# Kernel optimization log

Hardware: AMD Instinct MI355X
Metric: run time of the kernel (lower is better)

## Reference

```python
import jax, jax.numpy as jnp
import numpy as np

B, S, D, H, DK, DV, DFF = 8, 1024, 512, 8, 64, 64, 2048
EPS = 1e-6
NEG = -1e10


def _ln(x, w, b):
    # LayerNorm over last two dims ([S, D]) as in nn.LayerNorm([seq_len, d_model])
    m = jnp.mean(x, axis=(-2, -1), keepdims=True)
    v = jnp.var(x, axis=(-2, -1), keepdims=True)
    return (x - m) / jnp.sqrt(v + EPS) * w + b


def _mha(q, k, v, wq, bq, wk, bk, wv, bv, wo, bo, mask):
    # batched version of the per-head loop: wq/wk [H, D, DK], wv [H, D, DV]
    qh = jnp.einsum('bsd,hdk->bhsk', q, wq) + bq[:, None, :]
    kh = jnp.einsum('bsd,hdk->bhsk', k, wk) + bk[:, None, :]
    vh = jnp.einsum('bsd,hdv->bhsv', v, wv) + bv[:, None, :]
    sc = jnp.einsum('bhqk,bhmk->bhqm', qh, kh) / jnp.asarray(np.sqrt(DK), jnp.float32)
    sc = jnp.where(mask[:, None, None, :] == 0, NEG, sc)  # mask over key dim
    a = jax.nn.softmax(sc, axis=-1)
    o = jnp.einsum('bhqm,bhmv->bhqv', a, vh)
    o = o.transpose(0, 2, 1, 3).reshape(q.shape[0], q.shape[1], H * DV)
    return o @ wo.T + bo


def setup_inputs() -> dict:
    key = jax.random.key(0)
    ks = jax.random.split(key, 24)

    def w(k, shape):
        return (jax.random.normal(k, shape, jnp.float32) * 0.02)

    inp = {
        'x': jax.random.normal(ks[0], (B, S, D), jnp.float32),
        'y': jax.random.normal(ks[1], (B, S, D), jnp.float32),
        'src_mask': jax.random.randint(ks[2], (B, S), 0, 2, jnp.int32),
        'trg_mask': jax.random.randint(ks[3], (B, S), 0, 2, jnp.int32),
    }
    i = 4
    for pre in ('m1', 'm2'):
        inp[pre + '_wq'] = w(ks[i], (H, D, DK)); i += 1
        inp[pre + '_bq'] = jnp.zeros((H, DK), jnp.float32)
        inp[pre + '_wk'] = w(ks[i], (H, D, DK)); i += 1
        inp[pre + '_bk'] = jnp.zeros((H, DK), jnp.float32)
        inp[pre + '_wv'] = w(ks[i], (H, D, DV)); i += 1
        inp[pre + '_bv'] = jnp.zeros((H, DV), jnp.float32)
        inp[pre + '_wo'] = w(ks[i], (D, H * DV)); i += 1
        inp[pre + '_bo'] = jnp.zeros((D,), jnp.float32)
    inp['pw1'] = w(ks[i], (DFF, D)); i += 1
    inp['pb1'] = jnp.zeros((DFF,), jnp.float32)
    inp['pw2'] = w(ks[i], (D, DFF)); i += 1
    inp['pb2'] = jnp.zeros((D,), jnp.float32)
    for n in ('ln1', 'ln2', 'ln3'):
        inp[n + '_w'] = jnp.ones((S, D), jnp.float32)
        inp[n + '_b'] = jnp.zeros((S, D), jnp.float32)
    return inp


def reference(x, y, src_mask, trg_mask,
              m1_wq, m1_bq, m1_wk, m1_bk, m1_wv, m1_bv, m1_wo, m1_bo,
              m2_wq, m2_bq, m2_wk, m2_bk, m2_wv, m2_bv, m2_wo, m2_bo,
              pw1, pb1, pw2, pb2,
              ln1_w, ln1_b, ln2_w, ln2_b, ln3_w, ln3_b):
    # self-attention + residual + LN (dropout is identity at eval)
    h = _mha(x, x, x, m1_wq, m1_bq, m1_wk, m1_bk, m1_wv, m1_bv, m1_wo, m1_bo, trg_mask)
    x1 = _ln(x + h, ln1_w, ln1_b)
    # cross-attention
    h = _mha(x1, y, y, m2_wq, m2_bq, m2_wk, m2_bk, m2_wv, m2_bv, m2_wo, m2_bo, src_mask)
    x2 = _ln(x1 + h, ln2_w, ln2_b)
    # position-wise FFN
    ff = jax.nn.relu(x2 @ pw1.T + pb1) @ pw2.T + pb2
    return _ln(x2 + ff, ln3_w, ln3_b)
```

## Files before the change

### kernel.cpp

```cpp
#include <hip/hip_runtime.h>
#include <hip/hip_bf16.h>

#define B_   8
#define S_   1024
#define D_   512
#define H_   8
#define DK_  64
#define DFF_ 2048

typedef __hip_bfloat16 bf16;
typedef __attribute__((ext_vector_type(8))) short bf16x8;
typedef __attribute__((ext_vector_type(4))) float f32x4;

__device__ __forceinline__ float ldmix(const void* p, size_t i, int f) {
    return f ? __bfloat162float(((const bf16*)p)[i]) : ((const float*)p)[i];
}
__device__ __forceinline__ void store_o(float* p, float v) { *p = v; }
__device__ __forceinline__ void store_o(bf16* p, float v)  { *p = __float2bfloat16(v); }

__device__ __forceinline__ void gl_lds16(const void* g, void* l) {
    __builtin_amdgcn_global_load_lds(
        (const __attribute__((address_space(1))) unsigned int*)g,
        (__attribute__((address_space(3))) unsigned int*)l, 16, 0, 0);
}

__global__ __launch_bounds__(64) void detect_k(const unsigned short* __restrict__ x,
                                               float* __restrict__ stats,
                                               int* __restrict__ flag)
{
    if (threadIdx.x < 48) stats[threadIdx.x] = 0.f;
    int cnt = 0;
    for (int i = threadIdx.x; i < 4096; i += 64) {
        int e = (x[i] >> 7) & 0xFF;
        if (e >= 0xC0) cnt++;
    }
#pragma unroll
    for (int off = 32; off; off >>= 1) cnt += __shfl_xor(cnt, off);
    if (threadIdx.x == 0) { flag[0] = (cnt > 16) ? 0 : 1; flag[1] = 1; }
}

__global__ __launch_bounds__(256) void maskf_k(const int* __restrict__ trg,
                                               const int* __restrict__ src,
                                               float* __restrict__ trgf,
                                               float* __restrict__ srcf)
{
    int i = blockIdx.x * 256 + threadIdx.x;
    if (i < 8192) trgf[i] = trg[i] ? 0.f : -1.0e10f;
    else          srcf[i - 8192] = src[i - 8192] ? 0.f : -1.0e10f;
}

__global__ __launch_bounds__(256) void convxy_k(const void* __restrict__ x,
                                                const void* __restrict__ y,
                                                bf16* __restrict__ xb, bf16* __restrict__ yb,
                                                const int* __restrict__ flag)
{
    const int f = flag[0];
    const int N8 = 8192 * 512 / 8;
    int i = blockIdx.x * 256 + threadIdx.x;
    const void* src; bf16* dst; size_t base;
    if (i < N8) { src = x; dst = xb; base = (size_t)i * 8; }
    else        { src = y; dst = yb; base = (size_t)(i - N8) * 8; }
    if (f) {
        *(uint4*)(dst + base) = *(const uint4*)((const bf16*)src + base);
    } else {
        const float4 a = *(const float4*)((const float*)src + base);
        const float4 b = *(const float4*)((const float*)src + base + 4);
        bf16 o[8] = {__float2bfloat16(a.x), __float2bfloat16(a.y),
                     __float2bfloat16(a.z), __float2bfloat16(a.w),
                     __float2bfloat16(b.x), __float2bfloat16(b.y),
                     __float2bfloat16(b.z), __float2bfloat16(b.w)};
        *(uint4*)(dst + base) = *(uint4*)o;
    }
}

__global__ __launch_bounds__(256) void repack6_k(const void* __restrict__ w0, const void* __restrict__ w1,
                                                 const void* __restrict__ w2, const void* __restrict__ w3,
                                                 const void* __restrict__ w4, const void* __restrict__ w5,
                                                 bf16* __restrict__ out, const int* __restrict__ flag)
{
    const int f = flag[0];
    const int widx = blockIdx.x >> 10;
    const int j = ((blockIdx.x & 1023) << 8) + threadIdx.x;
    const void* in = widx == 0 ? w0 : widx == 1 ? w1 : widx == 2 ? w2
                   : widx == 3 ? w3 : widx == 4 ? w4 : w5;
    int n = j >> 9, d = j & 511;
    int h = n >> 6, k = n & 63;
    out[(size_t)widx * 262144 + j] =
        __float2bfloat16(ldmix(in, (size_t)h * (D_ * DK_) + (size_t)d * DK_ + k, f));
}

__global__ __launch_bounds__(256) void convw4_k(const void* __restrict__ wo1, const void* __restrict__ wo2,
                                                const void* __restrict__ pw1, const void* __restrict__ pw2,
                                                bf16* __restrict__ out, const int* __restrict__ flag)
{
    const int f = flag[0];
    const size_t i8 = (size_t)(blockIdx.x * 256 + threadIdx.x) * 8;
    const void* in; size_t off;
    if (i8 < 262144)       { in = wo1; off = 0; }
    else if (i8 < 524288)  { in = wo2; off = 262144; }
    else if (i8 < 1572864) { in = pw1; off = 524288; }
    else                   { in = pw2; off = 1572864; }
    const size_t s = i8 - off;
    if (f) {
        *(uint4*)(out + i8) = *(const uint4*)((const bf16*)in + s);
    } else {
        const float4 a = *(const float4*)((const float*)in + s);
        const float4 b = *(const float4*)((const float*)in + s + 4);
        bf16 o[8] = {__float2bfloat16(a.x), __float2bfloat16(a.y),
                     __float2bfloat16(a.z), __float2bfloat16(a.w),
                     __float2bfloat16(b.x), __float2bfloat16(b.y),
                     __float2bfloat16(b.z), __float2bfloat16(b.w)};
        *(uint4*)(out + i8) = *(uint4*)o;
    }
}

template <int NB>
__device__ __forceinline__ void gemm_core(const bf16* __restrict__ A, const bf16* __restrict__ Wt,
                                          int K, int m0, int n0, bf16* As, bf16* Bs,
                                          f32x4 (&acc)[4][NB])
{
    const int tid = threadIdx.x;
    const int lane = tid & 63, w = tid >> 6;
    const int wr = w >> 1, wc = w & 1;
    const int l16 = lane & 15, quad = lane >> 4;
    const int r0 = tid >> 2;
    const int g0 = (tid & 3) ^ ((r0 >> 1) & 3);
    const bf16* pa0 = A + (size_t)(m0 + r0) * K + g0 * 8;
    const bf16* pa1 = pa0 + (size_t)64 * K;
    const bf16* pb0 = Wt + (size_t)(n0 + r0) * K + g0 * 8;
    const bf16* pb1 = pb0 + (size_t)64 * K;
    bf16* lA0 = As + w * 512;
    bf16* lA1 = As + 2048 + w * 512;
    bf16* lB0 = Bs + w * 512;
    bf16* lB1 = Bs + 2048 + w * 512;

    int aoff[4], boff[NB];
#pragma unroll
    for (int i = 0; i < 4; ++i) {
        const int ra = wr * 64 + i * 16 + l16;
        aoff[i] = ra * 32 + (quad ^ ((ra >> 1) & 3)) * 8;
    }
#pragma unroll
    for (int j = 0; j < NB; ++j) {
        const int rb = wc * (NB * 16) + j * 16 + l16;
        boff[j] = rb * 32 + (quad ^ ((rb >> 1) & 3)) * 8;
    }

    for (int k0 = 0; k0 < K; k0 += 32) {
        __syncthreads();
        gl_lds16(pa0 + k0, lA0);
        gl_lds16(pa1 + k0, lA1);
        gl_lds16(pb0 + k0, lB0);
        if constexpr (NB == 4) gl_lds16(pb1 + k0, lB1);
        __syncthreads();
        bf16x8 af[4], bg[NB];
#pragma unroll
        for (int i = 0; i < 4; ++i) af[i] = *(const bf16x8*)&As[aoff[i]];
#pragma unroll
        for (int j = 0; j < NB; ++j) bg[j] = *(const bf16x8*)&Bs[boff[j]];
#pragma unroll
        for (int i = 0; i < 4; ++i)
#pragma unroll
            for (int j = 0; j < NB; ++j)
                acc[i][j] = __builtin_amdgcn_mfma_f32_16x16x32_bf16(af[i], bg[j], acc[i][j], 0, 0, 0);
    }
}

template <int NB, bool HAS_RES, bool RELU, bool STATS, typename OutT>
__global__ __launch_bounds__(256)
void mgemm_k(const bf16* __restrict__ A, const bf16* __restrict__ Wt,
             const void* __restrict__ bias, const void* __restrict__ res,
             OutT* __restrict__ C, int N, int K, int Gx,
             const int* __restrict__ bflag, const int* __restrict__ rflag,
             float* __restrict__ stats)
{
    __shared__ bf16 As[4096];
    __shared__ bf16 Bs[NB * 1024];
    const int lin = blockIdx.x;
    const int mt = (lin & 7) * 8 + (lin >> 3) / Gx;
    const int nt = (lin >> 3) % Gx;
    const int m0 = mt * 128, n0 = nt * (NB * 32);

    f32x4 acc[4][NB];
#pragma unroll
    for (int i = 0; i < 4; ++i)
#pragma unroll
        for (int j = 0; j < NB; ++j) acc[i][j] = (f32x4){0.f, 0.f, 0.f, 0.f};

    gemm_core<NB>(A, Wt, K, m0, n0, As, Bs, acc);

    const int tid = threadIdx.x;
    const int lane = tid & 63, w = tid >> 6;
    const int wr = w >> 1, wc = w & 1;
    const int l16 = lane & 15, quad = lane >> 4;
    const int bf = bflag[0];
    int rf = 0;
    if constexpr (HAS_RES) rf = rflag[0];

    float s = 0.f, s2 = 0.f;
#pragma unroll
    for (int i = 0; i < 4; ++i) {
        const int row = m0 + wr * 64 + i * 16 + quad * 4;
#pragma unroll
        for (int j = 0; j < NB; ++j) {
            const int col = n0 + wc * (NB * 16) + j * 16 + l16;
            const float bv = ldmix(bias, col, bf);
#pragma unroll
            for (int r = 0; r < 4; ++r) {
                float c = acc[i][j][r] + bv;
                if constexpr (RELU) c = fmaxf(c, 0.f);
                if constexpr (HAS_RES) c += ldmix(res, (size_t)(row + r) * N + col, rf);
                if constexpr (STATS) { s += c; s2 += c * c; }
                store_o(&C[(size_t)(row + r) * N + col], c);
            }
        }
    }
    if constexpr (STATS) {
#pragma unroll
        for (int off = 32; off; off >>= 1) { s += __shfl_xor(s, off); s2 += __shfl_xor(s2, off); }
        __syncthreads();
        float* red = (float*)As;
        if (lane == 0) { red[w * 2] = s; red[w * 2 + 1] = s2; }
        __syncthreads();
        if (tid == 0) {
            const int b = m0 >> 10;
            atomicAdd(&stats[b * 2],     red[0] + red[2] + red[4] + red[6]);
            atomicAdd(&stats[b * 2 + 1], red[1] + red[3] + red[5] + red[7]);
        }
    }
}

template <int NB, int RSHIFT>
__global__ __launch_bounds__(256)
void mgemm_qkv_k(const bf16* __restrict__ A, const bf16* __restrict__ Wbase,
                 const void* __restrict__ bq, const void* __restrict__ bk, const void* __restrict__ bv,
                 bf16* __restrict__ qout, bf16* __restrict__ kout, bf16* __restrict__ vtout,
                 int Gx, int roff, const int* __restrict__ bflag)
{
    __shared__ bf16 As[4096];
    __shared__ bf16 Bs[NB * 1024];
    const int lin = blockIdx.x;
    const int mt = (lin & 7) * 8 + (lin >> 3) / Gx;
    const int nt = (lin >> 3) % Gx;
    const int m0 = mt * 128, n0 = nt * (NB * 32);

    f32x4 acc[4][NB];
#pragma unroll
    for (int i = 0; i < 4; ++i)
#pragma unroll
        for (int j = 0; j < NB; ++j) acc[i][j] = (f32x4){0.f, 0.f, 0.f, 0.f};

    gemm_core<NB>(A, Wbase, 512, m0, n0, As, Bs, acc);

    const int tid = threadIdx.x;
    const int lane = tid & 63, w = tid >> 6;
    const int wr = w >> 1, wc = w & 1;
    const int l16 = lane & 15, quad = lane >> 4;
    const int bf = bflag[0];
    const int region = roff + (nt >> RSHIFT);
    const void* bptr = region == 0 ? bq : (region == 1 ? bk : bv);

#pragma unroll
    for (int i = 0; i < 4; ++i) {
        const int row = m0 + wr * 64 + i * 16 + quad * 4;
#pragma unroll
        for (int j = 0; j < NB; ++j) {
            const int col = n0 + wc * (NB * 16) + j * 16 + l16;
            const int colr = col & 511;
            const float bvv = ldmix(bptr, colr, bf);
#pragma unroll
            for (int r = 0; r < 4; ++r) {
                const int rr = row + r;
                float c = acc[i][j][r] + bvv;
                if (region == 0) {
                    qout[(size_t)rr * 512 + colr] = __float2bfloat16(c * 0.125f);
                } else if (region == 1) {
                    kout[(size_t)rr * 512 + colr] = __float2bfloat16(c);
                } else {
                    const int b = rr >> 10, key = rr & 1023;
                    vtout[((size_t)(b * 512 + colr) << 10) | key] = __float2bfloat16(c);
                }
            }
        }
    }
}

__global__ __launch_bounds__(256)
void mfattn_k(const bf16* __restrict__ Q, const bf16* __restrict__ Kb,
              const bf16* __restrict__ Vt, const float* __restrict__ maskf,
              bf16* __restrict__ O)
{
    const int lin = blockIdx.x;
    const int j = lin >> 3, xcd = lin & 7;
    const int head = xcd * 8 + (j >> 4);
    const int qt = j & 15;
    const int b = head >> 3, h = head & 7, s0 = qt * 64;
    const int tid = threadIdx.x;
    const int lane = tid & 63, w = tid >> 6;
    const int l16 = lane & 15, quad = lane >> 4;
    const int bS = b * S_, hc = h * DK_;
    const size_t vtb = (size_t)(b * H_ + h) * (DK_ * S_);

    __shared__ bf16 QPs[64 * 72];
    __shared__ bf16 Ks[64 * 72];
    __shared__ bf16 Vs[64 * 72];

    const int str = tid >> 3;
    const int stc = (tid & 7) * 8;

    *(uint4*)&QPs[str * 72 + stc]        = *(const uint4*)&Q[(size_t)(bS + s0 + str) * D_ + hc + stc];
    *(uint4*)&QPs[(str + 32) * 72 + stc] = *(const uint4*)&Q[(size_t)(bS + s0 + str + 32) * D_ + hc + stc];
    __syncthreads();

    const bf16x8 aq0 = *(const bf16x8*)&QPs[(w * 16 + l16) * 72 + quad * 8];
    const bf16x8 aq1 = *(const bf16x8*)&QPs[(w * 16 + l16) * 72 + quad * 8 + 32];

    f32x4 acc_o[4];
#pragma unroll
    for (int nb = 0; nb < 4; ++nb) acc_o[nb] = (f32x4){0.f, 0.f, 0.f, 0.f};
    float lrow[4] = {0.f, 0.f, 0.f, 0.f};

    for (int t0 = 0; t0 < S_; t0 += 64) {
        __syncthreads();
        *(uint4*)&Ks[str * 72 + stc]        = *(const uint4*)&Kb[(size_t)(bS + t0 + str) * D_ + hc + stc];
        *(uint4*)&Ks[(str + 32) * 72 + stc] = *(const uint4*)&Kb[(size_t)(bS + t0 + str + 32) * D_ + hc + stc];
        *(uint4*)&Vs[str * 72 + stc]        = *(const uint4*)&Vt[vtb + (size_t)str * S_ + t0 + stc];
        *(uint4*)&Vs[(str + 32) * 72 + stc] = *(const uint4*)&Vt[vtb + (size_t)(str + 32) * S_ + t0 + stc];
        __syncthreads();

        f32x4 sacc[4];
#pragma unroll
        for (int nb = 0; nb < 4; ++nb) sacc[nb] = (f32x4){0.f, 0.f, 0.f, 0.f};
#pragma unroll
        for (int nb = 0; nb < 4; ++nb) {
            const bf16x8 b0 = *(const bf16x8*)&Ks[(nb * 16 + l16) * 72 + quad * 8];
            const bf16x8 b1 = *(const bf16x8*)&Ks[(nb * 16 + l16) * 72 + quad * 8 + 32];
            sacc[nb] = __builtin_amdgcn_mfma_f32_16x16x32_bf16(aq0, b0, sacc[nb], 0, 0, 0);
            sacc[nb] = __builtin_amdgcn_mfma_f32_16x16x32_bf16(aq1, b1, sacc[nb], 0, 0, 0);
        }

#pragma unroll
        for (int nb = 0; nb < 4; ++nb) {
            const float mv = maskf[bS + t0 + nb * 16 + l16];
#pragma unroll
            for (int r = 0; r < 4; ++r) {
                const float p = __expf(sacc[nb][r] + mv);
                lrow[r] += p;
                QPs[(w * 16 + quad * 4 + r) * 72 + nb * 16 + l16] = __float2bfloat16(p);
            }
        }

        const bf16x8 ap0 = *(const bf16x8*)&QPs[(w * 16 + l16) * 72 + quad * 8];
        const bf16x8 ap1 = *(const bf16x8*)&QPs[(w * 16 + l16) * 72 + quad * 8 + 32];
#pragma unroll
        for (int nb = 0; nb < 4; ++nb) {
            const bf16x8 v0 = *(const bf16x8*)&Vs[(nb * 16 + l16) * 72 + quad * 8];
            const bf16x8 v1 = *(const bf16x8*)&Vs[(nb * 16 + l16) * 72 + quad * 8 + 32];
            acc_o[nb] = __builtin_amdgcn_mfma_f32_16x16x32_bf16(ap0, v0, acc_o[nb], 0, 0, 0);
            acc_o[nb] = __builtin_amdgcn_mfma_f32_16x16x32_bf16(ap1, v1, acc_o[nb], 0, 0, 0);
        }
    }

#pragma unroll
    for (int r = 0; r < 4; ++r) {
        float ls = lrow[r];
#pragma unroll
        for (int off = 8; off; off >>= 1) ls += __shfl_xor(ls, off);
        const float invl = 1.0f / ls;
        const size_t row = (size_t)(bS + s0 + w * 16 + quad * 4 + r) * D_;
#pragma unroll
        for (int nb = 0; nb < 4; ++nb)
            O[row + hc + nb * 16 + l16] = __float2bfloat16(acc_o[nb][r] * invl);
    }
}

template <bool FINAL>
__global__ __launch_bounds__(256)
void ln_apply_k(const float* __restrict__ Z, const float* __restrict__ stats,
                const void* __restrict__ w, const void* __restrict__ bb,
                bf16* __restrict__ outb, void* __restrict__ out_final,
                const int* __restrict__ flag)
{
    const int f = flag[0];
    const int b = blockIdx.y;
    const int i4 = (blockIdx.x * 256 + threadIdx.x) * 4;
    const float n = (float)(S_ * D_);
    const float m = stats[b * 2] / n;
    const float var = stats[b * 2 + 1] / n - m * m;
    const float inv = rsqrtf(var + 1e-6f);
    const size_t g = (size_t)b * (S_ * D_) + i4;
    const float4 z = *(const float4*)&Z[g];
    float v[4];
    v[0] = (z.x - m) * inv * ldmix(w, i4 + 0, f) + ldmix(bb, i4 + 0, f);
    v[1] = (z.y - m) * inv * ldmix(w, i4 + 1, f) + ldmix(bb, i4 + 1, f);
    v[2] = (z.z - m) * inv * ldmix(w, i4 + 2, f) + ldmix(bb, i4 + 2, f);
    v[3] = (z.w - m) * inv * ldmix(w, i4 + 3, f) + ldmix(bb, i4 + 3, f);
    union { ushort4 u4; unsigned short u[4]; } ov;
#pragma unroll
    for (int k = 0; k < 4; ++k) {
        bf16 t = __float2bfloat16(v[k]);
        __builtin_memcpy(&ov.u[k], &t, 2);
    }
    if constexpr (FINAL) {
        if (f) *(ushort4*)&((bf16*)out_final)[g] = ov.u4;
        else   *(float4*)&((float*)out_final)[g] = make_float4(v[0], v[1], v[2], v[3]);
    } else {
        *(ushort4*)&outb[g] = ov.u4;
    }
}

extern "C" void kernel_launch(void* const* d_in, const int* in_sizes, int n_in,
                              void* d_out, int out_size, void* d_ws, size_t ws_size,
                              hipStream_t stream)
{
    (void)in_sizes; (void)n_in; (void)out_size; (void)ws_size;

    const void* x        = d_in[0];
    const void* y        = d_in[1];
    const int*  src_mask = (const int*) d_in[2];
    const int*  trg_mask = (const int*) d_in[3];
    const void* m1_wq = d_in[4];
    const void* m1_bq = d_in[5];
    const void* m1_wk = d_in[6];
    const void* m1_bk = d_in[7];
    const void* m1_wv = d_in[8];
    const void* m1_bv = d_in[9];
    const void* m1_wo = d_in[10];
    const void* m1_bo = d_in[11];
    const void* m2_wq = d_in[12];
    const void* m2_bq = d_in[13];
    const void* m2_wk = d_in[14];
    const void* m2_bk = d_in[15];
    const void* m2_wv = d_in[16];
    const void* m2_bv = d_in[17];
    const void* m2_wo = d_in[18];
    const void* m2_bo = d_in[19];
    const void* pw1   = d_in[20];
    const void* pb1   = d_in[21];
    const void* pw2   = d_in[22];
    const void* pb2   = d_in[23];
    const void* ln1_w = d_in[24];
    const void* ln1_b = d_in[25];
    const void* ln2_w = d_in[26];
    const void* ln2_b = d_in[27];
    const void* ln3_w = d_in[28];
    const void* ln3_b = d_in[29];

    const size_t NACT = (size_t)8192 * 512;

    float* zb    = (float*)d_ws;
    float* stats = zb + NACT;
    int*   flag  = (int*)(stats + 48);
    float* trgf  = stats + 64;
    float* srcf  = trgf + 8192;
    bf16* xb16 = (bf16*)(srcf + 8192);
    bf16* yb16 = xb16 + NACT;
    bf16* qb   = yb16 + NACT;
    bf16* kb   = qb   + NACT;
    bf16* vbT  = kb   + NACT;
    bf16* aob  = vbT  + NACT;
    bf16* x1b  = aob  + NACT;
    bf16* x2b  = x1b  + NACT;
    bf16* ffb  = x2b  + NACT;
    bf16* Wq1r = ffb  + (size_t)8192 * 2048;
    bf16* Wq2r = Wq1r + 3 * 262144;
    bf16* Wo1b = Wq1r + 6 * 262144;
    bf16* Wo2b = Wo1b + 262144;
    bf16* W1b  = Wo2b + 262144;
    bf16* W2b  = W1b  + 1048576;

    detect_k<<<1, 64, 0, stream>>>((const unsigned short*)x, stats, flag);
    maskf_k<<<64, 256, 0, stream>>>(trg_mask, src_mask, trgf, srcf);
    convxy_k<<<4096, 256, 0, stream>>>(x, y, xb16, yb16, flag);
    repack6_k<<<6144, 256, 0, stream>>>(m1_wq, m1_wk, m1_wv, m2_wq, m2_wk, m2_wv, Wq1r, flag);
    convw4_k<<<1280, 256, 0, stream>>>(m1_wo, m2_wo, pw1, pw2, Wo1b, flag);

    const dim3 blk(256);
    const dim3 gln(512, B_);

    mgemm_qkv_k<4, 2><<<dim3(12 * 64), blk, 0, stream>>>(xb16, Wq1r, m1_bq, m1_bk, m1_bv, qb, kb, vbT, 12, 0, flag);
    mfattn_k<<<dim3(1024), blk, 0, stream>>>(qb, kb, vbT, trgf, aob);
    mgemm_k<2, true, false, true, float><<<dim3(8 * 64), blk, 0, stream>>>(aob, Wo1b, m1_bo, x, zb, 512, 512, 8, flag, flag, stats);
    ln_apply_k<false><<<gln, blk, 0, stream>>>(zb, stats, ln1_w, ln1_b, x1b, nullptr, flag);

    mgemm_qkv_k<2, 3><<<dim3(8 * 64), blk, 0, stream>>>(x1b, Wq2r, m2_bq, m2_bk, m2_bv, qb, kb, vbT, 8, 0, flag);
    mgemm_qkv_k<4, 2><<<dim3(8 * 64), blk, 0, stream>>>(yb16, Wq2r + 262144, m2_bq, m2_bk, m2_bv, qb, kb, vbT, 8, 1, flag);
    mfattn_k<<<dim3(1024), blk, 0, stream>>>(qb, kb, vbT, srcf, aob);
    mgemm_k<2, true, false, true, float><<<dim3(8 * 64), blk, 0, stream>>>(aob, Wo2b, m2_bo, x1b, zb, 512, 512, 8, flag, flag + 1, stats + 16);
    ln_apply_k<false><<<gln, blk, 0, stream>>>(zb, stats + 16, ln2_w, ln2_b, x2b, nullptr, flag);

    mgemm_k<4, false, true, false, bf16><<<dim3(16 * 64), blk, 0, stream>>>(x2b, W1b, pb1, nullptr, ffb, 2048, 512, 16, flag, flag, nullptr);
    mgemm_k<2, true, false, true, float><<<dim3(8 * 64), blk, 0, stream>>>(ffb, W2b, pb2, x2b, zb, 512, 2048, 8, flag, flag + 1, stats + 32);
    ln_apply_k<true><<<gln, blk, 0, stream>>>(zb, stats + 32, ln3_w, ln3_b, nullptr, d_out, flag);
}
```

Measured before the change: 522.2 us.

## Multi-buffer GEMM LDS tiles with async prefetch and vmcnt waits

Turns the single-buffered GEMM K-loop into a double or triple-buffered pipeline. Tiles are prefetched via global_load_lds one or two steps ahead, and explicit s_waitcnt vmcnt counts gate the barriers. This overlaps global-to-LDS transfer with MFMA work instead of stalling on two __syncthreads per K step. It costs two or three times the LDS per block, which may lower occupancy, and relies on exact hand-counted waitcnt values.

```diff
diff --git a/kernel.cpp b/kernel.cpp
--- a/kernel.cpp
+++ b/kernel.cpp
@@ -23,6 +23,9 @@
         (const __attribute__((address_space(1))) unsigned int*)g,
         (__attribute__((address_space(3))) unsigned int*)l, 16, 0, 0);
 }
+
+#define WAITV(N)  asm volatile("s_waitcnt vmcnt(" #N ")" ::: "memory")
+#define WAITLGKM0 asm volatile("s_waitcnt lgkmcnt(0)" ::: "memory")
 
 __global__ __launch_bounds__(64) void detect_k(const unsigned short* __restrict__ x,
                                                float* __restrict__ stats,
@@ -119,6 +122,8 @@
                                           int K, int m0, int n0, bf16* As, bf16* Bs,
                                           f32x4 (&acc)[4][NB])
 {
+    constexpr int PF   = (NB == 2) ? 2 : 1;
+    constexpr int NBUF = PF + 1;
     const int tid = threadIdx.x;
     const int lane = tid & 63, w = tid >> 6;
     const int wr = w >> 1, wc = w & 1;
@@ -129,10 +134,6 @@
     const bf16* pa1 = pa0 + (size_t)64 * K;
     const bf16* pb0 = Wt + (size_t)(n0 + r0) * K + g0 * 8;
     const bf16* pb1 = pb0 + (size_t)64 * K;
-    bf16* lA0 = As + w * 512;
-    bf16* lA1 = As + 2048 + w * 512;
-    bf16* lB0 = Bs + w * 512;
-    bf16* lB1 = Bs + 2048 + w * 512;
 
     int aoff[4], boff[NB];
 #pragma unroll
@@ -146,23 +147,50 @@
         boff[j] = rb * 32 + (quad ^ ((rb >> 1) & 3)) * 8;
     }
 
-    for (int k0 = 0; k0 < K; k0 += 32) {
-        __syncthreads();
-        gl_lds16(pa0 + k0, lA0);
-        gl_lds16(pa1 + k0, lA1);
-        gl_lds16(pb0 + k0, lB0);
-        if constexpr (NB == 4) gl_lds16(pb1 + k0, lB1);
-        __syncthreads();
+    auto stage = [&](int bi, int k0) {
+        bf16* a = As + bi * 4096;
+        bf16* b = Bs + bi * (NB * 1024);
+        gl_lds16(pa0 + k0, a + w * 512);
+        gl_lds16(pa1 + k0, a + 2048 + w * 512);
+        gl_lds16(pb0 + k0, b + w * 512);
+        if constexpr (NB == 4) gl_lds16(pb1 + k0, b + 2048 + w * 512);
+    };
+
+    const int NT = K >> 5;
+    stage(0, 0);
+    if constexpr (PF == 2) stage(1, 32);
+    int cur = 0, nxt = PF;
+
+    for (int t = 0; t < NT; ++t) {
+        if (t + PF < NT) {
+            stage(nxt, (t + PF) << 5);
+            if constexpr (NB == 4) WAITV(4); else WAITV(6);
+        } else if (t + 1 < NT) {
+            WAITV(3);
+        } else {
+            WAITV(0);
+        }
+        __builtin_amdgcn_s_barrier();
+        __builtin_amdgcn_sched_barrier(0);
+
+        const bf16* Ab = As + cur * 4096;
+        const bf16* Bb = Bs + cur * (NB * 1024);
         bf16x8 af[4], bg[NB];
 #pragma unroll
-        for (int i = 0; i < 4; ++i) af[i] = *(const bf16x8*)&As[aoff[i]];
-#pragma unroll
-        for (int j = 0; j < NB; ++j) bg[j] = *(const bf16x8*)&Bs[boff[j]];
+        for (int i = 0; i < 4; ++i) af[i] = *(const bf16x8*)&Ab[aoff[i]];
+#pragma unroll
+        for (int j = 0; j < NB; ++j) bg[j] = *(const bf16x8*)&Bb[boff[j]];
 #pragma unroll
         for (int i = 0; i < 4; ++i)
 #pragma unroll
             for (int j = 0; j < NB; ++j)
                 acc[i][j] = __builtin_amdgcn_mfma_f32_16x16x32_bf16(af[i], bg[j], acc[i][j], 0, 0, 0);
+
+        WAITLGKM0;
+        __builtin_amdgcn_sched_barrier(0);
+        __builtin_amdgcn_s_barrier();
+        cur = (cur + 1 == NBUF) ? 0 : cur + 1;
+        nxt = (nxt + 1 == NBUF) ? 0 : nxt + 1;
     }
 }
 
@@ -174,8 +202,9 @@
              const int* __restrict__ bflag, const int* __restrict__ rflag,
              float* __restrict__ stats)
 {
-    __shared__ bf16 As[4096];
-    __shared__ bf16 Bs[NB * 1024];
+    constexpr int NBUF = (NB == 2) ? 3 : 2;
+    __shared__ bf16 As[NBUF * 4096];
+    __shared__ bf16 Bs[NBUF * NB * 1024];
     const int lin = blockIdx.x;
     const int mt = (lin & 7) * 8 + (lin >> 3) / Gx;
     const int nt = (lin >> 3) % Gx;
@@ -237,8 +266,9 @@
                  bf16* __restrict__ qout, bf16* __restrict__ kout, bf16* __restrict__ vtout,
                  int Gx, int roff, const int* __restrict__ bflag)
 {
-    __shared__ bf16 As[4096];
-    __shared__ bf16 Bs[NB * 1024];
+    constexpr int NBUF = (NB == 2) ? 3 : 2;
+    __shared__ bf16 As[NBUF * 4096];
+    __shared__ bf16 Bs[NBUF * NB * 1024];
     const int lin = blockIdx.x;
     const int mt = (lin & 7) * 8 + (lin >> 3) / Gx;
     const int nt = (lin >> 3) % Gx;
```

Result: no change. 515.9 us, median of 2 (-1.2%).
